# Kernel tuning notes

Measured on AMD Instinct MI355X. Metric: run time of the kernel, lower is better.

The kernel has to match this reference:

```python
import jax, jax.numpy as jnp
import numpy as np

NQ = 23          # num_qubits = arch[-1]
NL = 2           # n_layers = len(arch) - 1
IN_DIM = 1024
ARCH0 = 23       # arch[0]


def _apply_1q(state, gate, q):
    # state: flat [2**NQ] complex; qubit q is bit q (little-endian, Qiskit convention)
    s = state.reshape(-1, 2, 2 ** q)
    return jnp.einsum('ab,xbj->xaj', gate, s).reshape(-1)


def _cnot_adjacent(state, q):
    # CNOT control=q, target=q+1: flip bit (q+1) where bit q == 1
    s = state.reshape(-1, 2, 2, 2 ** q)  # axes: [high, bit q+1, bit q, low]
    out = jnp.stack([s[:, :, 0, :], s[:, ::-1, 1, :]], axis=2)
    return out.reshape(-1)


def _ry(theta):
    c, s = jnp.cos(theta / 2), jnp.sin(theta / 2)
    return jnp.array(0, jnp.complex64) + jnp.stack(
        [jnp.stack([c, -s]), jnp.stack([s, c])])


def _rx(theta):
    c, s = jnp.cos(theta / 2), jnp.sin(theta / 2)
    i = jnp.array(1j, jnp.complex64)
    return jnp.stack([jnp.stack([c + 0j, -i * s]), jnp.stack([-i * s, c + 0j])]).astype(jnp.complex64)


def _rz(phi):
    e = jnp.exp(-1j * phi.astype(jnp.complex64) / 2)
    z = jnp.zeros((), jnp.complex64)
    return jnp.stack([jnp.stack([e, z]), jnp.stack([z, jnp.conj(e)])])


def setup_inputs() -> dict:
    key = jax.random.key(0)
    k1, k2, k3 = jax.random.split(key, 3)
    x = jax.random.normal(k1, (IN_DIM,), dtype=jnp.float32)
    W = jax.random.normal(k2, (ARCH0, IN_DIM), dtype=jnp.float32) / np.sqrt(IN_DIM)
    q_params = jax.random.normal(k3, (NL * NQ * 2,), dtype=jnp.float32)
    return {"x": x, "W": W, "q_params": q_params}


def reference(x, W, q_params):
    # classical part: h = tanh(Linear(x)) (no bias)
    h = jnp.tanh(W @ x)                       # [ARCH0]
    angles = h[:NQ]

    # statevector |0...0>
    state = jnp.zeros(2 ** NQ, jnp.complex64).at[0].set(1.0)

    # input encoding: RY(2 * h_i) on qubit i
    for q in range(NQ):
        state = _apply_1q(state, _ry(2.0 * angles[q]), q)

    # variational layers
    for layer in range(NL):
        for q in range(NQ):
            idx = layer * NQ * 2 + q * 2
            state = _apply_1q(state, _rx(q_params[idx]), q)
            state = _apply_1q(state, _rz(q_params[idx + 1]), q)
        for q in range(NQ - 1):
            state = _cnot_adjacent(state, q)

    # expectation of Pauli-Z on qubit 0 (bit 0 = last axis of reshape(-1, 2))
    probs = (state.real ** 2 + state.imag ** 2).reshape(-1, 2)
    exp_val = (probs[:, 0] - probs[:, 1]).sum().astype(jnp.float32)
    return h, exp_val
```

## Files before the change

kernel.cpp:

```cpp
#include <hip/hip_runtime.h>
#include <math.h>

#define NQ 23
#define IN_DIM 1024

__device__ inline void apply_gate_q(float* re, float* im, int q,
                                    float g00r, float g00i, float g01r, float g01i,
                                    float g10r, float g10i, float g11r, float g11i)
{
    const int stride = 1 << q;
    for (int b = 0; b < 2; ++b) {
        const int i0 = (q == 0) ? (b * 2) : b;
        const int i1 = i0 + stride;
        const float ar = re[i0], ai = im[i0];
        const float br = re[i1], bi = im[i1];
        re[i0] = g00r * ar - g00i * ai + g01r * br - g01i * bi;
        im[i0] = g00r * ai + g00i * ar + g01r * bi + g01i * br;
        re[i1] = g10r * ar - g10i * ai + g11r * br - g11i * bi;
        im[i1] = g10r * ai + g10i * ar + g11r * bi + g11i * br;
    }
}

__global__ __launch_bounds__(1024)
void qnn_kernel(const float* __restrict__ x,
                const float* __restrict__ W,
                const float* __restrict__ qp,
                float* __restrict__ out)
{
    const int t    = threadIdx.x;
    const int lane = t & 63;
    const int wave = t >> 6;

    __shared__ float partial[NQ][16];
    __shared__ float hsh[2];

    const float xv = x[t];
    #pragma unroll 1
    for (int r = 0; r < NQ; ++r) {
        float v = W[r * IN_DIM + t] * xv;
        v += __shfl_xor(v, 32, 64);
        v += __shfl_xor(v, 16, 64);
        v += __shfl_xor(v,  8, 64);
        v += __shfl_xor(v,  4, 64);
        v += __shfl_xor(v,  2, 64);
        v += __shfl_xor(v,  1, 64);
        if (lane == 0) partial[r][wave] = v;
    }
    __syncthreads();

    if (t < NQ) {
        float s = 0.f;
        #pragma unroll
        for (int w = 0; w < 16; ++w) s += partial[t][w];
        const float h = tanhf(s);
        out[t] = h;
        if (t < 2) hsh[t] = h;
    }
    __syncthreads();

    if (t == 0) {
        float re[4] = {1.f, 0.f, 0.f, 0.f};
        float im[4] = {0.f, 0.f, 0.f, 0.f};

        for (int q = 0; q < 2; ++q) {
            const float h = hsh[q];
            const float c = cosf(h), s = sinf(h);
            apply_gate_q(re, im, q,
                         c, 0.f, -s, 0.f,
                         s, 0.f,  c, 0.f);
        }

        for (int layer = 0; layer < 2; ++layer) {
            for (int q = 0; q < 2; ++q) {
                const int idx = layer * NQ * 2 + q * 2;
                {
                    const float th = qp[idx] * 0.5f;
                    const float c = cosf(th), s = sinf(th);
                    apply_gate_q(re, im, q,
                                 c, 0.f, 0.f, -s,
                                 0.f, -s, c, 0.f);
                }
                {
                    const float ph = qp[idx + 1] * 0.5f;
                    const float c = cosf(ph), s = sinf(ph);
                    apply_gate_q(re, im, q,
                                 c, -s, 0.f, 0.f,
                                 0.f, 0.f, c, s);
                }
            }
            {
                float tr = re[1], ti = im[1];
                re[1] = re[3]; im[1] = im[3];
                re[3] = tr;    im[3] = ti;
            }
        }

        const float expv = (re[0] * re[0] + im[0] * im[0])
                         - (re[1] * re[1] + im[1] * im[1])
                         + (re[2] * re[2] + im[2] * im[2])
                         - (re[3] * re[3] + im[3] * im[3]);
        out[NQ] = expv;
    }
}

extern "C" void kernel_launch(void* const* d_in, const int* in_sizes, int n_in,
                              void* d_out, int out_size, void* d_ws, size_t ws_size,
                              hipStream_t stream)
{
    const float* x  = (const float*)d_in[0];
    const float* W  = (const float*)d_in[1];
    const float* qp = (const float*)d_in[2];
    float* out = (float*)d_out;

    qnn_kernel<<<1, 1024, 0, stream>>>(x, W, qp, out);
}
```

Before: 69.73 us.

## Split GEMV rows across blocks with float4 loads and separate simulation block

Launches one 256-thread block per output row of W, each using float4 loads and a single wave reduction, instead of one block looping over all rows. An extra block recomputes the first two rows itself and runs the four-amplitude simulation, so no inter-block sync is needed. This targets the serial row loop's latency in the single-block version, at the cost of duplicating two row dot-products.

```diff
diff --git a/kernel.cpp b/kernel.cpp
--- a/kernel.cpp
+++ b/kernel.cpp
@@ -21,7 +21,23 @@
     }
 }
 
-__global__ __launch_bounds__(1024)
+__device__ inline float dot4(float4 a, float4 b)
+{
+    return a.x * b.x + a.y * b.y + a.z * b.z + a.w * b.w;
+}
+
+__device__ inline float wave_reduce(float v)
+{
+    v += __shfl_xor(v, 32, 64);
+    v += __shfl_xor(v, 16, 64);
+    v += __shfl_xor(v,  8, 64);
+    v += __shfl_xor(v,  4, 64);
+    v += __shfl_xor(v,  2, 64);
+    v += __shfl_xor(v,  1, 64);
+    return v;
+}
+
+__global__ __launch_bounds__(256)
 void qnn_kernel(const float* __restrict__ x,
                 const float* __restrict__ W,
                 const float* __restrict__ qp,
@@ -30,33 +46,36 @@
     const int t    = threadIdx.x;
     const int lane = t & 63;
     const int wave = t >> 6;
+    const int b    = blockIdx.x;
 
-    __shared__ float partial[NQ][16];
+    __shared__ float partial[4];
     __shared__ float hsh[2];
 
-    const float xv = x[t];
-    #pragma unroll 1
-    for (int r = 0; r < NQ; ++r) {
-        float v = W[r * IN_DIM + t] * xv;
-        v += __shfl_xor(v, 32, 64);
-        v += __shfl_xor(v, 16, 64);
-        v += __shfl_xor(v,  8, 64);
-        v += __shfl_xor(v,  4, 64);
-        v += __shfl_xor(v,  2, 64);
-        v += __shfl_xor(v,  1, 64);
-        if (lane == 0) partial[r][wave] = v;
+    const float4* __restrict__ x4 = (const float4*)x;
+    const float4* __restrict__ W4 = (const float4*)W;
+
+    const float4 xv = x4[t];
+
+    if (b < NQ) {
+        const float4 w = W4[b * 256 + t];
+        float v = wave_reduce(dot4(w, xv));
+        if (lane == 0) partial[wave] = v;
+        __syncthreads();
+        if (t == 0)
+            out[b] = tanhf(partial[0] + partial[1] + partial[2] + partial[3]);
+        return;
     }
-    __syncthreads();
 
-    if (t < NQ) {
-        float s = 0.f;
-        #pragma unroll
-        for (int w = 0; w < 16; ++w) s += partial[t][w];
-        const float h = tanhf(s);
-        out[t] = h;
-        if (t < 2) hsh[t] = h;
+    #pragma unroll
+    for (int r = 0; r < 2; ++r) {
+        const float4 w = W4[r * 256 + t];
+        float v = wave_reduce(dot4(w, xv));
+        if (lane == 0) partial[wave] = v;
+        __syncthreads();
+        if (t == 0)
+            hsh[r] = tanhf(partial[0] + partial[1] + partial[2] + partial[3]);
+        __syncthreads();
     }
-    __syncthreads();
 
     if (t == 0) {
         float re[4] = {1.f, 0.f, 0.f, 0.f};
@@ -89,7 +108,7 @@
                 }
             }
             {
-                float tr = re[1], ti = im[1];
+                const float tr = re[1], ti = im[1];
                 re[1] = re[3]; im[1] = im[3];
                 re[3] = tr;    im[3] = ti;
             }
@@ -112,5 +131,5 @@
     const float* qp = (const float*)d_in[2];
     float* out = (float*)d_out;
 
-    qnn_kernel<<<1, 1024, 0, stream>>>(x, W, qp, out);
+    qnn_kernel<<<NQ + 1, 256, 0, stream>>>(x, W, qp, out);
 }
```

After: 60.37 us. 13.4% less time.
